# Kernel tuning notes

Hardware: AMD Instinct MI355X
Metric: run time of the kernel (lower is better)

Reference implementation:

```python
import jax, jax.numpy as jnp
import numpy as np

B, D, H, E = 32768, 128, 512, 16

def setup_inputs() -> dict:
    key = jax.random.key(0)
    ks = jax.random.split(key, 5)
    x = jax.random.normal(ks[0], (B, 1, D), dtype=jnp.float32)
    s1 = 1.0 / float(np.sqrt(H))   # init_ uses last-dim size: w1 last dim = H
    s2 = 1.0 / float(np.sqrt(D))   # w2 last dim = D
    sg = 1.0 / float(np.sqrt(D))   # nn.Linear(D, E) default init scale
    w1 = jax.random.uniform(ks[1], (E, D, H), minval=-s1, maxval=s1, dtype=jnp.float32)
    w2 = jax.random.uniform(ks[2], (E, H, D), minval=-s2, maxval=s2, dtype=jnp.float32)
    wg = jax.random.uniform(ks[3], (D, E), minval=-sg, maxval=sg, dtype=jnp.float32)
    bg = jax.random.uniform(ks[4], (E,), minval=-sg, maxval=sg, dtype=jnp.float32)
    return {"x": x, "w1": w1, "w2": w2, "wg": wg, "bg": bg}

def reference(x, w1, w2, wg, bg):
    xt = x[:, 0, :]                                   # (B, D); seq dim is 1 by construction
    logits = xt @ wg + bg                             # (B, E)
    topk_vals, topk_idx = jax.lax.top_k(logits, 1)    # (B, 1) each
    scores = jax.nn.softmax(topk_vals, axis=-1)       # (B, 1); all ones for k=1
    # every expert processes every token (faithful to the reference)
    hidden = jax.nn.gelu(jnp.einsum('bd,edh->ebh', xt, w1), approximate=False)  # (E, B, H)
    eout = jnp.einsum('ebh,ehd->ebd', hidden, w2)     # (E, B, D)
    # gather selected expert per token, scale, sum over k
    sel = jnp.take_along_axis(eout.transpose(1, 0, 2), topk_idx[:, :, None], axis=1)  # (B, 1, D)
    return (sel * scores[:, :, None]).sum(axis=1)     # (B, D)
```

## Files before the change

kernel.cpp:

```cpp
#include <hip/hip_runtime.h>
#include <hip/hip_bf16.h>
#include <math.h>

#define NB 32768
#define DD 128
#define HH 512
#define EE 16
#define TM 64
#define HC 64
#define NCH (HH / HC)

typedef __attribute__((ext_vector_type(8))) short short8;
typedef __attribute__((ext_vector_type(4))) float f32x4;
typedef __attribute__((address_space(1))) const unsigned short gc_us;
typedef __attribute__((address_space(3))) unsigned short lds_us;

__device__ __forceinline__ unsigned short f2bf(float f) {
  union { float f; unsigned u; } v; v.f = f;
  unsigned r = v.u + 0x7fffu + ((v.u >> 16) & 1u);
  return (unsigned short)(r >> 16);
}

__device__ __forceinline__ float fast_erf(float z) {
  float a = fabsf(z);
  float t = __builtin_amdgcn_rcpf(1.0f + 0.3275911f * a);
  float y = t * (0.254829592f + t * (-0.284496736f + t * (1.421413741f +
            t * (-1.453152027f + t * 1.061405429f))));
  float r = 1.0f - y * __expf(-a * a);
  return z < 0.0f ? -r : r;
}

__global__ __launch_bounds__(256) void prep_kernel(
    const float* __restrict__ x, const float* __restrict__ wg,
    const float* __restrict__ bg, const float* __restrict__ w1,
    const float* __restrict__ w2, int* __restrict__ counts,
    int* __restrict__ rows, unsigned short* __restrict__ w1T,
    unsigned short* __restrict__ w2T) {
  __shared__ __align__(16) char smem[50816];
  int tid = threadIdx.x;

  if (blockIdx.x >= 512) {
    float (*tile)[65] = (float (*)[65])smem;
    int tp = blockIdx.x - 512;
    const float* src; unsigned short* dst; int S, Sd;
    if (tp < 256) {
      int e = tp >> 4, t2 = tp & 15;
      int d0 = (t2 >> 3) * 64, h0 = (t2 & 7) * 64;
      src = w1 + (size_t)e * DD * HH + (size_t)d0 * HH + h0; S = HH;
      dst = w1T + (size_t)e * HH * DD + (size_t)h0 * DD + d0; Sd = DD;
    } else {
      int t = tp - 256;
      int e = t >> 4, t2 = t & 15;
      int h0 = (t2 >> 1) * 64, d0 = (t2 & 1) * 64;
      src = w2 + (size_t)e * HH * DD + (size_t)h0 * DD + d0; S = DD;
      dst = w2T + (size_t)e * DD * HH + (size_t)d0 * HH + h0; Sd = HH;
    }
    #pragma unroll
    for (int i = 0; i < 4; ++i) {
      int u = tid + i * 256, r = u >> 4, c = (u & 15) * 4;
      float4 v = *(const float4*)(src + (size_t)r * S + c);
      tile[r][c + 0] = v.x; tile[r][c + 1] = v.y;
      tile[r][c + 2] = v.z; tile[r][c + 3] = v.w;
    }
    __syncthreads();
    #pragma unroll
    for (int i = 0; i < 4; ++i) {
      int u = tid + i * 256, tr = u >> 4, tc = (u & 15) * 4;
      ushort4 p;
      p.x = f2bf(tile[tc + 0][tr]); p.y = f2bf(tile[tc + 1][tr]);
      p.z = f2bf(tile[tc + 2][tr]); p.w = f2bf(tile[tc + 3][tr]);
      *(ushort4*)(dst + (size_t)tr * Sd + tc) = p;
    }
    return;
  }

  float  (*sx)[132] = (float (*)[132])smem;
  double (*swg)[EE] = (double (*)[EE])(smem + 33792);
  int* lcnt  = (int*)(smem + 50176);
  int* gbase = lcnt + EE;
  int* lslot = gbase + EE;
  int* lexp  = lslot + 64;

  int base = blockIdx.x * 64;
  if (tid < EE) lcnt[tid] = 0;
  for (int i = tid; i < DD * EE; i += 256) swg[i >> 4][i & 15] = (double)wg[i];
  {
    int r = tid >> 2, c0 = (tid & 3) * 32;
    const float4* src = (const float4*)(x + (size_t)(base + r) * DD + c0);
    #pragma unroll
    for (int i = 0; i < 8; ++i)
      *(float4*)&sx[r][c0 + i * 4] = src[i];
  }
  __syncthreads();

  int r = tid >> 2;
  int e0 = (tid & 3) * 4;
  double acc[4];
  #pragma unroll
  for (int j = 0; j < 4; ++j) acc[j] = (double)bg[e0 + j];

  #pragma unroll 4
  for (int d = 0; d < DD; ++d) {
    double xv = (double)sx[r][d];
    #pragma unroll
    for (int j = 0; j < 4; ++j)
      acc[j] += xv * swg[d][e0 + j];
  }

  int beste = 0; double bestv = acc[0];
  #pragma unroll
  for (int j = 1; j < 4; ++j)
    if (acc[j] > bestv) { bestv = acc[j]; beste = j; }
  int ge = e0 + beste;

  #pragma unroll
  for (int off = 1; off < 4; off <<= 1) {
    double ov = __shfl_xor(bestv, off);
    int oe = __shfl_xor(ge, off);
    if (ov > bestv || (ov == bestv && oe < ge)) { bestv = ov; ge = oe; }
  }

  if ((tid & 3) == 0) {
    lslot[r] = atomicAdd(&lcnt[ge], 1);
    lexp[r] = ge;
  }
  __syncthreads();
  if (tid < EE && lcnt[tid] > 0)
    gbase[tid] = atomicAdd(&counts[tid], lcnt[tid]);
  __syncthreads();
  if ((tid & 3) == 0) {
    int e2 = lexp[r];
    rows[e2 * NB + gbase[e2] + lslot[r]] = base + r;
  }
}

__global__ __launch_bounds__(256, 2) void moe_gemm(
    const float* __restrict__ x, const unsigned short* __restrict__ w1T,
    const unsigned short* __restrict__ w2T, const int* __restrict__ counts,
    const int* __restrict__ rows, float* __restrict__ out) {
  int e = blockIdx.x;
  int cnt = counts[e];
  int base = blockIdx.y * TM;
  if (base >= cnt) return;

  __shared__ unsigned short sW1[2][HC * DD];
  __shared__ unsigned short sW2[2][DD * HC];
  __shared__ unsigned short sH[TM][72];

  int tid = threadIdx.x;
  int wv = tid >> 6, l = tid & 63;
  int lm = l & 15, q = l >> 4;

  const unsigned short* w1e = w1T + (size_t)e * HH * DD;
  const unsigned short* w2e = w2T + (size_t)e * DD * HH;

  short8 xa[4];
  {
    int ridx = base + wv * 16 + lm; if (ridx >= cnt) ridx = cnt - 1;
    int grow = rows[e * NB + ridx];
    const float* xr = x + (size_t)grow * DD + q * 8;
    #pragma unroll
    for (int ks = 0; ks < 4; ++ks) {
      f32x4 v0 = *(const f32x4*)(xr + ks * 32);
      f32x4 v1 = *(const f32x4*)(xr + ks * 32 + 4);
      short8 a;
      a[0] = f2bf(v0[0]); a[1] = f2bf(v0[1]); a[2] = f2bf(v0[2]); a[3] = f2bf(v0[3]);
      a[4] = f2bf(v1[0]); a[5] = f2bf(v1[1]); a[6] = f2bf(v1[2]); a[7] = f2bf(v1[3]);
      xa[ks] = a;
    }
  }

  auto stage_chunk = [&](int buf, int c) {
    const unsigned short* w1c = w1e + (size_t)c * HC * DD;
    const unsigned short* w2c = w2e + (size_t)c * HC;
    #pragma unroll
    for (int i = 0; i < 4; ++i) {
      int r = wv * 16 + i * 4 + (l >> 4);
      const unsigned short* g = w1c + (size_t)r * DD + (((l & 15) ^ (r & 7)) << 3);
      __builtin_amdgcn_global_load_lds((gc_us*)g,
          (lds_us*)(&sW1[buf][wv * 2048 + i * 512]), 16, 0, 0);
    }
    #pragma unroll
    for (int i = 0; i < 4; ++i) {
      int r = wv * 32 + i * 8 + (l >> 3);
      const unsigned short* g = w2c + (size_t)r * HH + (((l & 7) ^ (r & 7)) << 3);
      __builtin_amdgcn_global_load_lds((gc_us*)g,
          (lds_us*)(&sW2[buf][wv * 2048 + i * 512]), 16, 0, 0);
    }
  };

  stage_chunk(0, 0);
  __syncthreads();

  f32x4 acc2[8];
  #pragma unroll
  for (int n = 0; n < 8; ++n) acc2[n] = (f32x4){0.f, 0.f, 0.f, 0.f};

  for (int hc = 0; hc < NCH; ++hc) {
    int b = hc & 1;

    if (hc + 1 < NCH) stage_chunk(b ^ 1, hc + 1);

    f32x4 acc1[4];
    #pragma unroll
    for (int n = 0; n < 4; ++n) acc1[n] = (f32x4){0.f, 0.f, 0.f, 0.f};
    #pragma unroll
    for (int ks = 0; ks < 4; ++ks) {
      #pragma unroll
      for (int n = 0; n < 4; ++n) {
        int row = n * 16 + lm;
        int sl = ((ks * 4 + q) ^ (row & 7)) * 8;
        short8 bfr = *(const short8*)&sW1[b][row * DD + sl];
        acc1[n] = __builtin_amdgcn_mfma_f32_16x16x32_bf16(xa[ks], bfr, acc1[n], 0, 0, 0);
      }
    }
    #pragma unroll
    for (int n = 0; n < 4; ++n) {
      #pragma unroll
      for (int rr = 0; rr < 4; ++rr) {
        float v = acc1[n][rr];
        float g = 0.5f * v * (1.0f + fast_erf(v * 0.70710678118654752f));
        sH[wv * 16 + q * 4 + rr][n * 16 + lm] = f2bf(g);
      }
    }
    #pragma unroll
    for (int ks = 0; ks < 2; ++ks) {
      int kk = ks * 32 + q * 8;
      short8 a = *(const short8*)&sH[wv * 16 + lm][kk];
      #pragma unroll
      for (int n = 0; n < 8; ++n) {
        int row = n * 16 + lm;
        int sl = ((ks * 4 + q) ^ (row & 7)) * 8;
        short8 bfr = *(const short8*)&sW2[b][row * HC + sl];
        acc2[n] = __builtin_amdgcn_mfma_f32_16x16x32_bf16(a, bfr, acc2[n], 0, 0, 0);
      }
    }

    __syncthreads();
  }

  #pragma unroll
  for (int rr = 0; rr < 4; ++rr) {
    int ml = wv * 16 + q * 4 + rr;
    int ridx = base + ml;
    if (ridx < cnt) {
      int grow = rows[e * NB + ridx];
      float* op = out + (size_t)grow * DD + lm;
      #pragma unroll
      for (int n = 0; n < 8; ++n) op[n * 16] = acc2[n][rr];
    }
  }
}

extern "C" void kernel_launch(void* const* d_in, const int* in_sizes, int n_in,
                              void* d_out, int out_size, void* d_ws, size_t ws_size,
                              hipStream_t stream) {
  const float* x  = (const float*)d_in[0];
  const float* w1 = (const float*)d_in[1];
  const float* w2 = (const float*)d_in[2];
  const float* wg = (const float*)d_in[3];
  const float* bg = (const float*)d_in[4];
  float* out = (float*)d_out;

  int* counts = (int*)d_ws;
  int* rows   = (int*)((char*)d_ws + 1024);
  unsigned short* w1T = (unsigned short*)((char*)d_ws + 1024 + (size_t)EE * NB * 4);
  unsigned short* w2T = w1T + (size_t)EE * HH * DD;

  hipMemsetAsync(d_ws, 0, 64, stream);
  hipLaunchKernelGGL(prep_kernel, dim3(1024), dim3(256), 0, stream,
                     x, wg, bg, w1, w2, counts, rows, w1T, w2T);
  hipLaunchKernelGGL(moe_gemm, dim3(EE, NB / TM), dim3(256), 0, stream,
                     x, w1T, w2T, counts, rows, out);
}
```

Baseline: 135.2 us.

## Halve token tile, split hidden chunk across waves with split-K reduction

Shrinks the token tile from 64 to 32 rows and has pairs of waves split each 64-wide hidden chunk (hf halves) with a final LDS split-K reduction of the second GEMM's accumulators. The weight double buffer is removed in favour of a single buffer with a sync after each load, cutting LDS so launch bounds can request 4 blocks per CU. This gives more blocks and higher occupancy and reduces padding waste for partially filled expert tiles. In exchange, weight traffic per token doubles and the load/compute overlap inside a block is lost, leaving other resident blocks to hide latency.

Measured after the change: 129.5 us. 4.2% less time.

```diff
diff --git a/kernel.cpp b/kernel.cpp
--- a/kernel.cpp
+++ b/kernel.cpp
@@ -6,7 +6,7 @@
 #define DD 128
 #define HH 512
 #define EE 16
-#define TM 64
+#define TM 32
 #define HC 64
 #define NCH (HH / HC)
 
@@ -134,7 +134,7 @@
   }
 }
 
-__global__ __launch_bounds__(256, 2) void moe_gemm(
+__global__ __launch_bounds__(256, 4) void moe_gemm(
     const float* __restrict__ x, const unsigned short* __restrict__ w1T,
     const unsigned short* __restrict__ w2T, const int* __restrict__ counts,
     const int* __restrict__ rows, float* __restrict__ out) {
@@ -143,20 +143,22 @@
   int base = blockIdx.y * TM;
   if (base >= cnt) return;
 
-  __shared__ unsigned short sW1[2][HC * DD];
-  __shared__ unsigned short sW2[2][DD * HC];
-  __shared__ unsigned short sH[TM][72];
+  __shared__ __align__(16) unsigned short sW1[HC * DD];
+  __shared__ __align__(16) unsigned short sW2[DD * HC];
+  __shared__ __align__(16) unsigned short sH[TM * 80];
 
   int tid = threadIdx.x;
   int wv = tid >> 6, l = tid & 63;
   int lm = l & 15, q = l >> 4;
+  int rg = wv & 1;
+  int hf = wv >> 1;
 
   const unsigned short* w1e = w1T + (size_t)e * HH * DD;
   const unsigned short* w2e = w2T + (size_t)e * DD * HH;
 
   short8 xa[4];
   {
-    int ridx = base + wv * 16 + lm; if (ridx >= cnt) ridx = cnt - 1;
+    int ridx = base + rg * 16 + lm; if (ridx >= cnt) ridx = cnt - 1;
     int grow = rows[e * NB + ridx];
     const float* xr = x + (size_t)grow * DD + q * 8;
     #pragma unroll
@@ -170,84 +172,87 @@
     }
   }
 
-  auto stage_chunk = [&](int buf, int c) {
-    const unsigned short* w1c = w1e + (size_t)c * HC * DD;
-    const unsigned short* w2c = w2e + (size_t)c * HC;
-    #pragma unroll
-    for (int i = 0; i < 4; ++i) {
-      int r = wv * 16 + i * 4 + (l >> 4);
-      const unsigned short* g = w1c + (size_t)r * DD + (((l & 15) ^ (r & 7)) << 3);
-      __builtin_amdgcn_global_load_lds((gc_us*)g,
-          (lds_us*)(&sW1[buf][wv * 2048 + i * 512]), 16, 0, 0);
-    }
-    #pragma unroll
-    for (int i = 0; i < 4; ++i) {
-      int r = wv * 32 + i * 8 + (l >> 3);
-      const unsigned short* g = w2c + (size_t)r * HH + (((l & 7) ^ (r & 7)) << 3);
-      __builtin_amdgcn_global_load_lds((gc_us*)g,
-          (lds_us*)(&sW2[buf][wv * 2048 + i * 512]), 16, 0, 0);
-    }
-  };
-
-  stage_chunk(0, 0);
-  __syncthreads();
-
   f32x4 acc2[8];
   #pragma unroll
   for (int n = 0; n < 8; ++n) acc2[n] = (f32x4){0.f, 0.f, 0.f, 0.f};
 
   for (int hc = 0; hc < NCH; ++hc) {
-    int b = hc & 1;
-
-    if (hc + 1 < NCH) stage_chunk(b ^ 1, hc + 1);
-
-    f32x4 acc1[4];
-    #pragma unroll
-    for (int n = 0; n < 4; ++n) acc1[n] = (f32x4){0.f, 0.f, 0.f, 0.f};
+    {
+      const unsigned short* w1c = w1e + (size_t)hc * HC * DD;
+      const unsigned short* w2c = w2e + (size_t)hc * HC;
+      #pragma unroll
+      for (int i = 0; i < 4; ++i) {
+        int r = wv * 16 + i * 4 + (l >> 4);
+        const unsigned short* g = w1c + (size_t)r * DD + (((l & 15) ^ (r & 7)) << 3);
+        __builtin_amdgcn_global_load_lds((gc_us*)g,
+            (lds_us*)(&sW1[wv * 2048 + i * 512]), 16, 0, 0);
+      }
+      #pragma unroll
+      for (int i = 0; i < 4; ++i) {
+        int r = wv * 32 + i * 8 + (l >> 3);
+        const unsigned short* g = w2c + (size_t)r * HH + (((l & 7) ^ (r & 7)) << 3);
+        __builtin_amdgcn_global_load_lds((gc_us*)g,
+            (lds_us*)(&sW2[wv * 2048 + i * 512]), 16, 0, 0);
+      }
+    }
+    __syncthreads();
+
+    f32x4 acc1[2];
+    #pragma unroll
+    for (int n = 0; n < 2; ++n) acc1[n] = (f32x4){0.f, 0.f, 0.f, 0.f};
     #pragma unroll
     for (int ks = 0; ks < 4; ++ks) {
       #pragma unroll
-      for (int n = 0; n < 4; ++n) {
-        int row = n * 16 + lm;
+      for (int n = 0; n < 2; ++n) {
+        int row = hf * 32 + n * 16 + lm;
         int sl = ((ks * 4 + q) ^ (row & 7)) * 8;
-        short8 bfr = *(const short8*)&sW1[b][row * DD + sl];
+        short8 bfr = *(const short8*)&sW1[row * DD + sl];
         acc1[n] = __builtin_amdgcn_mfma_f32_16x16x32_bf16(xa[ks], bfr, acc1[n], 0, 0, 0);
       }
     }
     #pragma unroll
-    for (int n = 0; n < 4; ++n) {
+    for (int n = 0; n < 2; ++n) {
       #pragma unroll
       for (int rr = 0; rr < 4; ++rr) {
         float v = acc1[n][rr];
         float g = 0.5f * v * (1.0f + fast_erf(v * 0.70710678118654752f));
-        sH[wv * 16 + q * 4 + rr][n * 16 + lm] = f2bf(g);
-      }
-    }
-    #pragma unroll
-    for (int ks = 0; ks < 2; ++ks) {
-      int kk = ks * 32 + q * 8;
-      short8 a = *(const short8*)&sH[wv * 16 + lm][kk];
+        sH[(rg * 16 + q * 4 + rr) * 80 + hf * 32 + n * 16 + lm] = f2bf(g);
+      }
+    }
+    {
+      short8 a = *(const short8*)&sH[(rg * 16 + lm) * 80 + hf * 32 + q * 8];
       #pragma unroll
       for (int n = 0; n < 8; ++n) {
         int row = n * 16 + lm;
-        int sl = ((ks * 4 + q) ^ (row & 7)) * 8;
-        short8 bfr = *(const short8*)&sW2[b][row * HC + sl];
+        int sl = ((hf * 4 + q) ^ (row & 7)) * 8;
+        short8 bfr = *(const short8*)&sW2[row * HC + sl];
         acc2[n] = __builtin_amdgcn_mfma_f32_16x16x32_bf16(a, bfr, acc2[n], 0, 0, 0);
       }
     }
-
     __syncthreads();
   }
 
-  #pragma unroll
-  for (int rr = 0; rr < 4; ++rr) {
-    int ml = wv * 16 + q * 4 + rr;
-    int ridx = base + ml;
-    if (ridx < cnt) {
-      int grow = rows[e * NB + ridx];
-      float* op = out + (size_t)grow * DD + lm;
-      #pragma unroll
-      for (int n = 0; n < 8; ++n) op[n * 16] = acc2[n][rr];
+  float* sc = (rg == 0) ? (float*)sW1 : (float*)sW2;
+  if (hf == 1) {
+    #pragma unroll
+    for (int n = 0; n < 8; ++n)
+      #pragma unroll
+      for (int rr = 0; rr < 4; ++rr)
+        sc[(q * 4 + rr) * 132 + n * 16 + lm] = acc2[n][rr];
+  }
+  __syncthreads();
+  if (hf == 0) {
+    #pragma unroll
+    for (int rr = 0; rr < 4; ++rr) {
+      int ml = rg * 16 + q * 4 + rr;
+      int ridx = base + ml;
+      if (ridx < cnt) {
+        int grow = rows[e * NB + ridx];
+        float* op = out + (size_t)grow * DD + lm;
+        #pragma unroll
+        for (int n = 0; n < 8; ++n)
+          op[n * 16] = acc2[n][rr] + sc[(q * 4 + rr) * 132 + n * 16 + lm];
+      }
     }
   }
 }
```

## Pre-pack weights into MFMA fragment layout and drop LDS staging

Applied to the files above, without the earlier changes.

The prep kernel now writes both expert weight matrices as bf16 in a packed layout that matches the 32x32x16 MFMA operand fragments, so each lane loads its fragment directly from global memory with one 16-byte read. The GEMM kernel switches from 16x16x32 to 32x32x16 MFMA with 2 waves of 32 rows per block. It removes LDS double buffering, LDS round trips for the hidden activations and the per-chunk barriers, and keeps the GELU outputs in registers as the A operand of the second GEMM. The trade-off is that every wave reads weights straight from global memory or cache without reuse across waves, and the prep transpose now does strided uncoalesced reads.

After: 139.7 us. 1.03x slower.

```diff
diff --git a/kernel.cpp b/kernel.cpp
--- a/kernel.cpp
+++ b/kernel.cpp
@@ -7,13 +7,10 @@
 #define HH 512
 #define EE 16
 #define TM 64
-#define HC 64
-#define NCH (HH / HC)
 
 typedef __attribute__((ext_vector_type(8))) short short8;
 typedef __attribute__((ext_vector_type(4))) float f32x4;
-typedef __attribute__((address_space(1))) const unsigned short gc_us;
-typedef __attribute__((address_space(3))) unsigned short lds_us;
+typedef __attribute__((ext_vector_type(16))) float f32x16;
 
 __device__ __forceinline__ unsigned short f2bf(float f) {
   union { float f; unsigned u; } v; v.f = f;
@@ -34,42 +31,42 @@
     const float* __restrict__ x, const float* __restrict__ wg,
     const float* __restrict__ bg, const float* __restrict__ w1,
     const float* __restrict__ w2, int* __restrict__ counts,
-    int* __restrict__ rows, unsigned short* __restrict__ w1T,
-    unsigned short* __restrict__ w2T) {
+    int* __restrict__ rows, unsigned short* __restrict__ wP) {
   __shared__ __align__(16) char smem[50816];
   int tid = threadIdx.x;
 
   if (blockIdx.x >= 512) {
-    float (*tile)[65] = (float (*)[65])smem;
-    int tp = blockIdx.x - 512;
-    const float* src; unsigned short* dst; int S, Sd;
-    if (tp < 256) {
-      int e = tp >> 4, t2 = tp & 15;
-      int d0 = (t2 >> 3) * 64, h0 = (t2 & 7) * 64;
-      src = w1 + (size_t)e * DD * HH + (size_t)d0 * HH + h0; S = HH;
-      dst = w1T + (size_t)e * HH * DD + (size_t)h0 * DD + d0; Sd = DD;
-    } else {
-      int t = tp - 256;
-      int e = t >> 4, t2 = t & 15;
-      int h0 = (t2 >> 1) * 64, d0 = (t2 & 1) * 64;
-      src = w2 + (size_t)e * HH * DD + (size_t)h0 * DD + d0; S = DD;
-      dst = w2T + (size_t)e * DD * HH + (size_t)d0 * HH + h0; Sd = HH;
-    }
-    #pragma unroll
-    for (int i = 0; i < 4; ++i) {
-      int u = tid + i * 256, r = u >> 4, c = (u & 15) * 4;
-      float4 v = *(const float4*)(src + (size_t)r * S + c);
-      tile[r][c + 0] = v.x; tile[r][c + 1] = v.y;
-      tile[r][c + 2] = v.z; tile[r][c + 3] = v.w;
-    }
-    __syncthreads();
-    #pragma unroll
-    for (int i = 0; i < 4; ++i) {
-      int u = tid + i * 256, tr = u >> 4, tc = (u & 15) * 4;
-      ushort4 p;
-      p.x = f2bf(tile[tc + 0][tr]); p.y = f2bf(tile[tc + 1][tr]);
-      p.z = f2bf(tile[tc + 2][tr]); p.w = f2bf(tile[tc + 3][tr]);
-      *(ushort4*)(dst + (size_t)tr * Sd + tc) = p;
+    int l = tid & 63, lc = l & 31, hi = l >> 5;
+    int gw = (blockIdx.x - 512) * 4 + (tid >> 6);
+    #pragma unroll
+    for (int i = 0; i < 2; ++i) {
+      int kb = gw * 2 + i;
+      int e = kb >> 8, v = kb & 255;
+      float vals[8];
+      if (v < 128) {
+        int hc = v >> 4, t = (v >> 3) & 1, ks = v & 7;
+        int h = hc * 64 + t * 32 + lc;
+        const float* src = w1 + (size_t)e * DD * HH + h;
+        int d0 = ks * 16 + hi * 8;
+        #pragma unroll
+        for (int j = 0; j < 8; ++j) vals[j] = src[(size_t)(d0 + j) * HH];
+      } else {
+        int b2 = v - 128;
+        int hc = b2 >> 4, s = (b2 >> 2) & 3, dt = b2 & 3;
+        int dout = dt * 32 + lc;
+        const float* src = w2 + (size_t)e * HH * DD + dout;
+        #pragma unroll
+        for (int j = 0; j < 8; ++j) {
+          int hp = hc * 64 + (s >> 1) * 32 + (j & 3) + 8 * ((s & 1) + 2 * (j >> 2)) + 4 * hi;
+          vals[j] = src[(size_t)hp * DD];
+        }
+      }
+      ushort4 p0, p1;
+      p0.x = f2bf(vals[0]); p0.y = f2bf(vals[1]); p0.z = f2bf(vals[2]); p0.w = f2bf(vals[3]);
+      p1.x = f2bf(vals[4]); p1.y = f2bf(vals[5]); p1.z = f2bf(vals[6]); p1.w = f2bf(vals[7]);
+      unsigned short* dst = wP + (size_t)kb * 512 + l * 8;
+      *(ushort4*)dst = p0;
+      *(ushort4*)(dst + 4) = p1;
     }
     return;
   }
@@ -134,35 +131,32 @@
   }
 }
 
-__global__ __launch_bounds__(256, 2) void moe_gemm(
-    const float* __restrict__ x, const unsigned short* __restrict__ w1T,
-    const unsigned short* __restrict__ w2T, const int* __restrict__ counts,
-    const int* __restrict__ rows, float* __restrict__ out) {
+__global__ __launch_bounds__(128, 2) void moe_gemm(
+    const float* __restrict__ x, const unsigned short* __restrict__ wP,
+    const int* __restrict__ counts, const int* __restrict__ rows,
+    float* __restrict__ out) {
   int e = blockIdx.x;
   int cnt = counts[e];
   int base = blockIdx.y * TM;
   if (base >= cnt) return;
 
-  __shared__ unsigned short sW1[2][HC * DD];
-  __shared__ unsigned short sW2[2][DD * HC];
-  __shared__ unsigned short sH[TM][72];
-
   int tid = threadIdx.x;
   int wv = tid >> 6, l = tid & 63;
-  int lm = l & 15, q = l >> 4;
-
-  const unsigned short* w1e = w1T + (size_t)e * HH * DD;
-  const unsigned short* w2e = w2T + (size_t)e * DD * HH;
-
-  short8 xa[4];
+  int lc = l & 31, hi = l >> 5;
+  int mb = base + wv * 32;
+  if (mb >= cnt) return;
+
+  const unsigned short* we = wP + (size_t)e * 256 * 512;
+
+  short8 xa[8];
   {
-    int ridx = base + wv * 16 + lm; if (ridx >= cnt) ridx = cnt - 1;
+    int ridx = mb + lc; if (ridx >= cnt) ridx = cnt - 1;
     int grow = rows[e * NB + ridx];
-    const float* xr = x + (size_t)grow * DD + q * 8;
-    #pragma unroll
-    for (int ks = 0; ks < 4; ++ks) {
-      f32x4 v0 = *(const f32x4*)(xr + ks * 32);
-      f32x4 v1 = *(const f32x4*)(xr + ks * 32 + 4);
+    const float* xr = x + (size_t)grow * DD + hi * 8;
+    #pragma unroll
+    for (int ks = 0; ks < 8; ++ks) {
+      f32x4 v0 = *(const f32x4*)(xr + ks * 16);
+      f32x4 v1 = *(const f32x4*)(xr + ks * 16 + 4);
       short8 a;
       a[0] = f2bf(v0[0]); a[1] = f2bf(v0[1]); a[2] = f2bf(v0[2]); a[3] = f2bf(v0[3]);
       a[4] = f2bf(v1[0]); a[5] = f2bf(v1[1]); a[6] = f2bf(v1[2]); a[7] = f2bf(v1[3]);
@@ -170,84 +164,56 @@
     }
   }
 
-  auto stage_chunk = [&](int buf, int c) {
-    const unsigned short* w1c = w1e + (size_t)c * HC * DD;
-    const unsigned short* w2c = w2e + (size_t)c * HC;
-    #pragma unroll
-    for (int i = 0; i < 4; ++i) {
-      int r = wv * 16 + i * 4 + (l >> 4);
-      const unsigned short* g = w1c + (size_t)r * DD + (((l & 15) ^ (r & 7)) << 3);
-      __builtin_amdgcn_global_load_lds((gc_us*)g,
-          (lds_us*)(&sW1[buf][wv * 2048 + i * 512]), 16, 0, 0);
-    }
-    #pragma unroll
-    for (int i = 0; i < 4; ++i) {
-      int r = wv * 32 + i * 8 + (l >> 3);
-      const unsigned short* g = w2c + (size_t)r * HH + (((l & 7) ^ (r & 7)) << 3);
-      __builtin_amdgcn_global_load_lds((gc_us*)g,
-          (lds_us*)(&sW2[buf][wv * 2048 + i * 512]), 16, 0, 0);
-    }
-  };
-
-  stage_chunk(0, 0);
-  __syncthreads();
-
-  f32x4 acc2[8];
-  #pragma unroll
-  for (int n = 0; n < 8; ++n) acc2[n] = (f32x4){0.f, 0.f, 0.f, 0.f};
-
-  for (int hc = 0; hc < NCH; ++hc) {
-    int b = hc & 1;
-
-    if (hc + 1 < NCH) stage_chunk(b ^ 1, hc + 1);
-
-    f32x4 acc1[4];
-    #pragma unroll
-    for (int n = 0; n < 4; ++n) acc1[n] = (f32x4){0.f, 0.f, 0.f, 0.f};
-    #pragma unroll
-    for (int ks = 0; ks < 4; ++ks) {
+  f32x16 acc2[4];
+  #pragma unroll
+  for (int dt = 0; dt < 4; ++dt)
+    #pragma unroll
+    for (int r = 0; r < 16; ++r) acc2[dt][r] = 0.f;
+
+  for (int hc = 0; hc < 8; ++hc) {
+    const unsigned short* wc1 = we + (size_t)hc * 16 * 512 + l * 8;
+    const unsigned short* wc2 = we + (size_t)(128 + hc * 16) * 512 + l * 8;
+    #pragma unroll
+    for (int t = 0; t < 2; ++t) {
+      f32x16 a1;
       #pragma unroll
-      for (int n = 0; n < 4; ++n) {
-        int row = n * 16 + lm;
-        int sl = ((ks * 4 + q) ^ (row & 7)) * 8;
-        short8 bfr = *(const short8*)&sW1[b][row * DD + sl];
-        acc1[n] = __builtin_amdgcn_mfma_f32_16x16x32_bf16(xa[ks], bfr, acc1[n], 0, 0, 0);
+      for (int r = 0; r < 16; ++r) a1[r] = 0.f;
+      #pragma unroll
+      for (int ks = 0; ks < 8; ++ks) {
+        short8 wf = *(const short8*)(wc1 + (t * 8 + ks) * 512);
+        a1 = __builtin_amdgcn_mfma_f32_32x32x16_bf16(wf, xa[ks], a1, 0, 0, 0);
       }
-    }
-    #pragma unroll
-    for (int n = 0; n < 4; ++n) {
       #pragma unroll
-      for (int rr = 0; rr < 4; ++rr) {
-        float v = acc1[n][rr];
-        float g = 0.5f * v * (1.0f + fast_erf(v * 0.70710678118654752f));
-        sH[wv * 16 + q * 4 + rr][n * 16 + lm] = f2bf(g);
+      for (int s2 = 0; s2 < 2; ++s2) {
+        short8 hf8;
+        #pragma unroll
+        for (int j = 0; j < 8; ++j) {
+          int r = (j & 3) | (s2 << 2) | ((j >> 2) << 3);
+          float v = a1[r];
+          float g = 0.5f * v * (1.0f + fast_erf(v * 0.70710678118654752f));
+          hf8[j] = (short)f2bf(g);
+        }
+        int s = 2 * t + s2;
+        #pragma unroll
+        for (int dt = 0; dt < 4; ++dt) {
+          short8 wf = *(const short8*)(wc2 + (s * 4 + dt) * 512);
+          acc2[dt] = __builtin_amdgcn_mfma_f32_32x32x16_bf16(hf8, wf, acc2[dt], 0, 0, 0);
+        }
       }
     }
-    #pragma unroll
-    for (int ks = 0; ks < 2; ++ks) {
-      int kk = ks * 32 + q * 8;
-      short8 a = *(const short8*)&sH[wv * 16 + lm][kk];
-      #pragma unroll
-      for (int n = 0; n < 8; ++n) {
-        int row = n * 16 + lm;
-        int sl = ((ks * 4 + q) ^ (row & 7)) * 8;
-        short8 bfr = *(const short8*)&sW2[b][row * HC + sl];
-        acc2[n] = __builtin_amdgcn_mfma_f32_16x16x32_bf16(a, bfr, acc2[n], 0, 0, 0);
-      }
-    }
-
-    __syncthreads();
-  }
-
-  #pragma unroll
-  for (int rr = 0; rr < 4; ++rr) {
-    int ml = wv * 16 + q * 4 + rr;
-    int ridx = base + ml;
+  }
+
+  #pragma unroll
+  for (int reg = 0; reg < 16; ++reg) {
+    int m = (reg & 3) + 8 * (reg >> 2) + 4 * hi;
+    int ridx = mb + m;
     if (ridx < cnt) {
       int grow = rows[e * NB + ridx];
-      float* op = out + (size_t)grow * DD + lm;
-      #pragma unroll
-      for (int n = 0; n < 8; ++n) op[n * 16] = acc2[n][rr];
+      float* op = out + (size_t)grow * DD + lc;
+      op[0]  = acc2[0][reg];
+      op[32] = acc2[1][reg];
+      op[64] = acc2[2][reg];
+      op[96] = acc2[3][reg];
     }
   }
 }
@@ -264,12 +230,11 @@
 
   int* counts = (int*)d_ws;
   int* rows   = (int*)((char*)d_ws + 1024);
-  unsigned short* w1T = (unsigned short*)((char*)d_ws + 1024 + (size_t)EE * NB * 4);
-  unsigned short* w2T = w1T + (size_t)EE * HH * DD;
+  unsigned short* wP = (unsigned short*)((char*)d_ws + 1024 + (size_t)EE * NB * 4);
 
   hipMemsetAsync(d_ws, 0, 64, stream);
   hipLaunchKernelGGL(prep_kernel, dim3(1024), dim3(256), 0, stream,
-                     x, wg, bg, w1, w2, counts, rows, w1T, w2T);
-  hipLaunchKernelGGL(moe_gemm, dim3(EE, NB / TM), dim3(256), 0, stream,
-                     x, w1T, w2T, counts, rows, out);
-}
+                     x, wg, bg, w1, w2, counts, rows, wP);
+  hipLaunchKernelGGL(moe_gemm, dim3(EE, NB / TM), dim3(128), 0, stream,
+                     x, wP, counts, rows, out);
+}
```
